# Kernel tuning notes

Hardware: AMD Instinct MI355X
Metric: run time of the kernel (lower is better)

## Reference

```python
import jax, jax.numpy as jnp
import numpy as np

B, L, D_IN = 8, 512, 1024
HEAD_SIZE = 64
NUM_LABELS = 16
INF = 1e12


def _rotary_sin_cos(seq_len, dim):
    # HF RoFormerSinusoidalPositionalEmbedding: inv_freq = 10000^(-2i/dim)
    pos = np.arange(seq_len, dtype=np.float64)[:, None]
    inv_freq = 1.0 / np.power(10000.0, 2.0 * np.arange(dim // 2) / dim)
    ang = pos * inv_freq  # [L, dim//2]
    # interleave: [s0, s0, s1, s1, ...] (matches stack([sin,sin],-1).reshape)
    sin = jnp.asarray(np.repeat(np.sin(ang), 2, axis=-1), dtype=jnp.float32)
    cos = jnp.asarray(np.repeat(np.cos(ang), 2, axis=-1), dtype=jnp.float32)
    return sin[None], cos[None]  # [1, L, dim]


def _rotate_half(x):
    # [-x1, x0, -x3, x2, ...]
    return jnp.stack([-x[..., 1::2], x[..., ::2]], axis=-1).reshape(x.shape)


def setup_inputs() -> dict:
    key = jax.random.key(0)
    k1, k2, k3, k4, k5 = jax.random.split(key, 5)
    s1 = 1.0 / np.sqrt(D_IN)
    s2 = 1.0 / np.sqrt(2 * HEAD_SIZE)
    return {
        "inputs": jax.random.normal(k1, (B, L, D_IN), dtype=jnp.float32),
        "attention_mask": jnp.ones((B, L), dtype=jnp.int32),
        "W1": jax.random.uniform(k2, (D_IN, 2 * HEAD_SIZE), jnp.float32, -s1, s1),
        "b1": jax.random.uniform(k3, (2 * HEAD_SIZE,), jnp.float32, -s1, s1),
        "W2": jax.random.uniform(k4, (2 * HEAD_SIZE, 2 * NUM_LABELS), jnp.float32, -s2, s2),
        "b2": jax.random.uniform(k5, (2 * NUM_LABELS,), jnp.float32, -s2, s2),
    }


def reference(inputs, attention_mask, W1, b1, W2, b2):
    h = inputs @ W1 + b1                      # [B, L, 2*head_size]
    qw, kw = h[..., ::2], h[..., 1::2]        # [B, L, head_size]

    sin, cos = _rotary_sin_cos(h.shape[1], HEAD_SIZE)
    qw = qw * cos + _rotate_half(qw) * sin
    kw = kw * cos + _rotate_half(kw) * sin

    logits = jnp.einsum("bmd,bnd->bmn", qw, kw) / (HEAD_SIZE ** 0.5)  # [B, L, L]

    bias = (h @ W2 + b2).transpose(0, 2, 1) / 2.0        # [B, 2*heads, L]
    logits = logits[:, None] + bias[:, ::2, None, :] + bias[:, 1::2, :, None]  # [B, heads, L, L]

    am = attention_mask.astype(logits.dtype)
    attn_mask = 1.0 - am[:, None, None, :] * am[:, None, :, None]
    logits = logits - attn_mask * INF

    tril = jnp.tril(jnp.ones((h.shape[1], h.shape[1]), logits.dtype), k=-1)
    logits = logits - tril * INF
    return logits
```

## Files before the change

kernel.cpp:

```cpp
#include <hip/hip_runtime.h>
#include <math.h>

#define B_   8
#define L_   512
#define DIN  1024
#define H_   128
#define HEAD 64
#define NL   16
#define INF_ 1.0e12f

#define SIN_OFF  0
#define COS_OFF  (512*32)
#define QROT_OFF (COS_OFF + 512*32)
#define KROT_OFF (QROT_OFF + B_*L_*HEAD)
#define BQ_OFF   (KROT_OFF + B_*L_*HEAD)
#define BK_OFF   (BQ_OFF + B_*NL*L_)
#define W1T_OFF  (BK_OFF + B_*NL*L_)
#define W2T_OFF  (W1T_OFF + 65536)

#define XSH_STRIDE 1032

typedef float          floatx4  __attribute__((ext_vector_type(4)));
typedef short          shortx8  __attribute__((ext_vector_type(8)));
typedef unsigned short ushortx8 __attribute__((ext_vector_type(8)));

__device__ __forceinline__ unsigned short f2bf(float f) {
    unsigned u = __float_as_uint(f);
    u += 0x7FFFu + ((u >> 16) & 1u);
    return (unsigned short)(u >> 16);
}

__global__ __launch_bounds__(256) void prep_kernel(const float* __restrict__ W1,
                                                   const float* __restrict__ W2,
                                                   float* __restrict__ ws) {
    __shared__ float lds[64 * 132];
    const int tid = threadIdx.x;
    const int bid = blockIdx.x;

    if (bid < 64) {
        int idx = bid * 256 + tid;
        int m = idx >> 5, i = idx & 31;
        float freq = expf(-(float)i * 0.28782313662425575f);
        float ang  = (float)m * freq;
        ws[SIN_OFF + idx] = sinf(ang);
        ws[COS_OFF + idx] = cosf(ang);
    } else if (bid < 80) {
        const int k0 = (bid - 64) * 64;
        for (int i = 0; i < 8; i++) {
            int f = tid + i * 256;
            int k = f >> 5, n4 = (f & 31) * 4;
            *(float4*)&lds[k * 132 + n4] = *(const float4*)&W1[(size_t)(k0 + k) * H_ + n4];
        }
        __syncthreads();
        unsigned short* W1T = (unsigned short*)(ws + W1T_OFF);
        const int n  = tid >> 1;
        const int kh = (tid & 1) * 32;
        for (int i = 0; i < 4; i++) {
            ushortx8 p;
            #pragma unroll
            for (int j = 0; j < 8; j++) p[j] = f2bf(lds[(kh + i * 8 + j) * 132 + n]);
            *(ushortx8*)&W1T[(size_t)n * DIN + k0 + kh + i * 8] = p;
        }
    } else {
        unsigned short* W2T = (unsigned short*)(ws + W2T_OFF);
        const int o  = tid >> 3;
        const int kc = (tid & 7) * 16;
        ushortx8 p0, p1;
        #pragma unroll
        for (int j = 0; j < 8; j++) p0[j] = f2bf(W2[(size_t)(kc + j) * 32 + o]);
        #pragma unroll
        for (int j = 0; j < 8; j++) p1[j] = f2bf(W2[(size_t)(kc + 8 + j) * 32 + o]);
        *(ushortx8*)&W2T[(size_t)o * H_ + kc]     = p0;
        *(ushortx8*)&W2T[(size_t)o * H_ + kc + 8] = p1;
    }
}

__global__ __launch_bounds__(1024, 2) void gemm1_fused_kernel(
    const float* __restrict__ X, const float* __restrict__ b1,
    const float* __restrict__ b2, float* __restrict__ ws)
{
    __shared__ __align__(16) float shbuf[8256];
    __shared__ float hs[16 * 132];

    unsigned short* Xsh = (unsigned short*)shbuf;
    float (*red)[16][64] = (float(*)[16][64])shbuf;

    const int tid  = threadIdx.x;
    const int m0   = blockIdx.x * 16;
    const int w    = tid >> 6;
    const int g    = w & 3;
    const int s    = w >> 2;
    const int lane = tid & 63;
    const int lrow = lane >> 4;
    const int lcol = lane & 15;

    const unsigned short* W1T = (const unsigned short*)(ws + W1T_OFF);

    const float* xrow = X + (size_t)(m0 + w) * DIN + lane * 8;
    float4 x0 = *(const float4*)(xrow + 0);
    float4 x1 = *(const float4*)(xrow + 4);
    float4 x2 = *(const float4*)(xrow + 512);
    float4 x3 = *(const float4*)(xrow + 516);

    const unsigned short* pB0 = W1T + (size_t)(g * 32 + lcol) * DIN + s * 256 + lrow * 8;
    const unsigned short* pB1 = pB0 + (size_t)16 * DIN;
    shortx8 bfr[16];
    #pragma unroll
    for (int st = 0; st < 8; st++) {
        bfr[2 * st]     = *(const shortx8*)(pB0 + st * 32);
        bfr[2 * st + 1] = *(const shortx8*)(pB1 + st * 32);
    }

    {
        ushortx8 ua, ub;
        ua[0] = f2bf(x0.x); ua[1] = f2bf(x0.y); ua[2] = f2bf(x0.z); ua[3] = f2bf(x0.w);
        ua[4] = f2bf(x1.x); ua[5] = f2bf(x1.y); ua[6] = f2bf(x1.z); ua[7] = f2bf(x1.w);
        ub[0] = f2bf(x2.x); ub[1] = f2bf(x2.y); ub[2] = f2bf(x2.z); ub[3] = f2bf(x2.w);
        ub[4] = f2bf(x3.x); ub[5] = f2bf(x3.y); ub[6] = f2bf(x3.z); ub[7] = f2bf(x3.w);
        *(ushortx8*)&Xsh[w * XSH_STRIDE + lane * 8]       = ua;
        *(ushortx8*)&Xsh[w * XSH_STRIDE + 512 + lane * 8] = ub;
    }
    __syncthreads();

    const unsigned short* pA = &Xsh[lcol * XSH_STRIDE + s * 256 + lrow * 8];

    floatx4 acc0 = {0.f, 0.f, 0.f, 0.f};
    floatx4 acc1 = {0.f, 0.f, 0.f, 0.f};

    #pragma unroll
    for (int st = 0; st < 8; st++) {
        shortx8 af = *(const shortx8*)(pA + st * 32);
        acc0 = __builtin_amdgcn_mfma_f32_16x16x32_bf16(af, bfr[2 * st],     acc0, 0, 0, 0);
        acc1 = __builtin_amdgcn_mfma_f32_16x16x32_bf16(af, bfr[2 * st + 1], acc1, 0, 0, 0);
    }
    __syncthreads();

    #pragma unroll
    for (int r = 0; r < 4; r++) {
        red[r][w][lane]     = acc0[r];
        red[4 + r][w][lane] = acc1[r];
    }
    __syncthreads();

    if (w < 4) {
        float b1a = b1[g * 32 + lcol];
        float b1b = b1[g * 32 + 16 + lcol];
        #pragma unroll
        for (int r = 0; r < 4; r++) {
            float v0 = red[r][g][lane]     + red[r][g + 4][lane]
                     + red[r][g + 8][lane] + red[r][g + 12][lane];
            float v1 = red[4 + r][g][lane]     + red[4 + r][g + 4][lane]
                     + red[4 + r][g + 8][lane] + red[4 + r][g + 12][lane];
            hs[(lrow * 4 + r) * 132 + g * 32 + lcol]      = v0 + b1a;
            hs[(lrow * 4 + r) * 132 + g * 32 + 16 + lcol] = v1 + b1b;
        }
    }
    __syncthreads();

    if (tid < 256) {
        int row = tid >> 4;
        int j   = tid & 15;
        int gg  = m0 + row;
        int pos = gg & (L_ - 1);
        const float* hr = &hs[row * 132];
        float h0 = hr[8 * j + 0], h1 = hr[8 * j + 1];
        float h2 = hr[8 * j + 2], h3 = hr[8 * j + 3];
        float h4 = hr[8 * j + 4], h5 = hr[8 * j + 5];
        float h6 = hr[8 * j + 6], h7 = hr[8 * j + 7];
        float s0 = ws[SIN_OFF + pos * 32 + 2 * j];
        float c0 = ws[COS_OFF + pos * 32 + 2 * j];
        float s1 = ws[SIN_OFF + pos * 32 + 2 * j + 1];
        float c1 = ws[COS_OFF + pos * 32 + 2 * j + 1];
        float4 q, k;
        q.x = h0 * c0 - h2 * s0;  q.y = h2 * c0 + h0 * s0;
        q.z = h4 * c1 - h6 * s1;  q.w = h6 * c1 + h4 * s1;
        k.x = h1 * c0 - h3 * s0;  k.y = h3 * c0 + h1 * s0;
        k.z = h5 * c1 - h7 * s1;  k.w = h7 * c1 + h5 * s1;
        *(float4*)&ws[QROT_OFF + (size_t)gg * HEAD + 4 * j] = q;
        *(float4*)&ws[KROT_OFF + (size_t)gg * HEAD + 4 * j] = k;
    }

    if (w == 0) {
        const unsigned short* W2T = (const unsigned short*)(ws + W2T_OFF);
        floatx4 bacc0 = {0.f, 0.f, 0.f, 0.f};
        floatx4 bacc1 = {0.f, 0.f, 0.f, 0.f};
        #pragma unroll
        for (int st = 0; st < 4; st++) {
            int k = st * 32 + lrow * 8;
            ushortx8 hfu;
            #pragma unroll
            for (int j = 0; j < 8; j++) hfu[j] = f2bf(hs[lcol * 132 + k + j]);
            shortx8 hf = (shortx8)hfu;
            shortx8 wf0 = *(const shortx8*)(W2T + (size_t)lcol * H_ + k);
            shortx8 wf1 = *(const shortx8*)(W2T + (size_t)(16 + lcol) * H_ + k);
            bacc0 = __builtin_amdgcn_mfma_f32_16x16x32_bf16(hf, wf0, bacc0, 0, 0, 0);
            bacc1 = __builtin_amdgcn_mfma_f32_16x16x32_bf16(hf, wf1, bacc1, 0, 0, 0);
        }
        float b2a = b2[lcol], b2b = b2[16 + lcol];
        #pragma unroll
        for (int r = 0; r < 4; r++) {
            int gg  = m0 + lrow * 4 + r;
            int bb  = gg >> 9;
            int pos = gg & (L_ - 1);
            float v0 = (bacc0[r] + b2a) * 0.5f;
            float v1 = (bacc1[r] + b2b) * 0.5f;
            int o0 = lcol, o1 = 16 + lcol;
            if (o0 & 1) ws[BQ_OFF + ((size_t)bb * NL + (o0 >> 1)) * L_ + pos] = v0;
            else        ws[BK_OFF + ((size_t)bb * NL + (o0 >> 1)) * L_ + pos] = v0;
            if (o1 & 1) ws[BQ_OFF + ((size_t)bb * NL + (o1 >> 1)) * L_ + pos] = v1;
            else        ws[BK_OFF + ((size_t)bb * NL + (o1 >> 1)) * L_ + pos] = v1;
        }
    }
}

__global__ __launch_bounds__(256) void qk_bcast_kernel(
    const int* __restrict__ am, const float* __restrict__ ws, float* __restrict__ out)
{
    __shared__ float Qs[64][68];
    __shared__ float Ks[64][68];
    __shared__ float BQs[16][64];
    __shared__ float BKs[16][64];
    __shared__ float maskM[64];
    __shared__ float maskN[64];

    const int tid = threadIdx.x;
    const int bid = blockIdx.x;
    const int bb = bid >> 6;
    const int mt = (bid >> 3) & 7;
    const int nt = bid & 7;
    const int m0 = mt * 64, n0 = nt * 64;

    {
        int r0   = tid >> 4;
        int dcol = (tid & 15) * 4;
        #pragma unroll
        for (int rr = 0; rr < 4; rr++) {
            int r = r0 + rr * 16;
            float4 q = *(const float4*)&ws[QROT_OFF + ((size_t)(bb * L_ + m0 + r)) * HEAD + dcol];
            float4 k = *(const float4*)&ws[KROT_OFF + ((size_t)(bb * L_ + n0 + r)) * HEAD + dcol];
            Qs[dcol + 0][r] = q.x; Qs[dcol + 1][r] = q.y;
            Qs[dcol + 2][r] = q.z; Qs[dcol + 3][r] = q.w;
            Ks[dcol + 0][r] = k.x; Ks[dcol + 1][r] = k.y;
            Ks[dcol + 2][r] = k.z; Ks[dcol + 3][r] = k.w;
        }
    }
    {
        int l = tid >> 4;
        int c = (tid & 15) * 4;
        *(float4*)&BQs[l][c] = *(const float4*)&ws[BQ_OFF + ((size_t)bb * NL + l) * L_ + m0 + c];
        *(float4*)&BKs[l][c] = *(const float4*)&ws[BK_OFF + ((size_t)bb * NL + l) * L_ + n0 + c];
    }
    if (tid < 64)       maskM[tid]      = (float)am[bb * L_ + m0 + tid];
    else if (tid < 128) maskN[tid - 64] = (float)am[bb * L_ + n0 + (tid - 64)];
    __syncthreads();

    const int ty = tid >> 4;
    const int tx = tid & 15;
    float acc[4][4] = {};
    #pragma unroll 8
    for (int d = 0; d < HEAD; d++) {
        float4 a  = *(const float4*)&Qs[d][ty * 4];
        float4 bv = *(const float4*)&Ks[d][tx * 4];
        acc[0][0] += a.x * bv.x; acc[0][1] += a.x * bv.y; acc[0][2] += a.x * bv.z; acc[0][3] += a.x * bv.w;
        acc[1][0] += a.y * bv.x; acc[1][1] += a.y * bv.y; acc[1][2] += a.y * bv.z; acc[1][3] += a.y * bv.w;
        acc[2][0] += a.z * bv.x; acc[2][1] += a.z * bv.y; acc[2][2] += a.z * bv.z; acc[2][3] += a.z * bv.w;
        acc[3][0] += a.w * bv.x; acc[3][1] += a.w * bv.y; acc[3][2] += a.w * bv.z; acc[3][3] += a.w * bv.w;
    }

    float4 base[4];
    #pragma unroll
    for (int r = 0; r < 4; r++) {
        int m = m0 + ty * 4 + r;
        float mm = maskM[ty * 4 + r];
        #pragma unroll
        for (int c = 0; c < 4; c++) {
            int n = n0 + tx * 4 + c;
            float v = acc[r][c] * 0.125f
                    - (1.0f - mm * maskN[tx * 4 + c]) * INF_
                    - ((n < m) ? INF_ : 0.0f);
            ((float*)&base[r])[c] = v;
        }
    }

    #pragma unroll
    for (int l = 0; l < NL; l++) {
        float4 bk4 = *(const float4*)&BKs[l][tx * 4];
        size_t outb = (((size_t)(bb * NL + l)) * L_ + m0 + ty * 4) * L_ + n0 + tx * 4;
        #pragma unroll
        for (int r = 0; r < 4; r++) {
            float bq = BQs[l][ty * 4 + r];
            float4 o;
            o.x = base[r].x + bk4.x + bq;
            o.y = base[r].y + bk4.y + bq;
            o.z = base[r].z + bk4.z + bq;
            o.w = base[r].w + bk4.w + bq;
            *(float4*)&out[outb + (size_t)r * L_] = o;
        }
    }
}

extern "C" void kernel_launch(void* const* d_in, const int* in_sizes, int n_in,
                              void* d_out, int out_size, void* d_ws, size_t ws_size,
                              hipStream_t stream) {
    const float* X  = (const float*)d_in[0];
    const int*   am = (const int*)d_in[1];
    const float* W1 = (const float*)d_in[2];
    const float* b1 = (const float*)d_in[3];
    const float* W2 = (const float*)d_in[4];
    const float* b2 = (const float*)d_in[5];
    float* out = (float*)d_out;
    float* ws  = (float*)d_ws;

    prep_kernel<<<81, 256, 0, stream>>>(W1, W2, ws);
    gemm1_fused_kernel<<<(B_ * L_) / 16, 1024, 0, stream>>>(X, b1, b2, ws);
    qk_bcast_kernel<<<B_ * (L_ / 64) * (L_ / 64), 256, 0, stream>>>(am, ws, out);
}
```

Measured before the change: 48.48 us.

## Split first GEMM into split-K partial kernel plus separate reduction epilogue

Replaces the single 1024-thread fused GEMM kernel with a 1024-block split-K kernel that writes partial sums to workspace. A new epilogue kernel sums the partials, adds bias, applies rotary, and computes the bias projection in FP32 from shared memory. This drops the W2 bf16 transpose from prep. The aim is more, smaller blocks for better occupancy, at the cost of an extra launch and a global round-trip for the partials.

New measurement: 55.72 us. 14.9% more time.

```diff
diff --git a/kernel.cpp b/kernel.cpp
--- a/kernel.cpp
+++ b/kernel.cpp
@@ -16,9 +16,7 @@
 #define BQ_OFF   (KROT_OFF + B_*L_*HEAD)
 #define BK_OFF   (BQ_OFF + B_*NL*L_)
 #define W1T_OFF  (BK_OFF + B_*NL*L_)
-#define W2T_OFF  (W1T_OFF + 65536)
-
-#define XSH_STRIDE 1032
+#define PART_OFF (W1T_OFF + 65536)
 
 typedef float          floatx4  __attribute__((ext_vector_type(4)));
 typedef short          shortx8  __attribute__((ext_vector_type(8)));
@@ -31,7 +29,6 @@
 }
 
 __global__ __launch_bounds__(256) void prep_kernel(const float* __restrict__ W1,
-                                                   const float* __restrict__ W2,
                                                    float* __restrict__ ws) {
     __shared__ float lds[64 * 132];
     const int tid = threadIdx.x;
@@ -44,7 +41,7 @@
         float ang  = (float)m * freq;
         ws[SIN_OFF + idx] = sinf(ang);
         ws[COS_OFF + idx] = cosf(ang);
-    } else if (bid < 80) {
+    } else {
         const int k0 = (bid - 64) * 64;
         for (int i = 0; i < 8; i++) {
             int f = tid + i * 256;
@@ -61,48 +58,35 @@
             for (int j = 0; j < 8; j++) p[j] = f2bf(lds[(kh + i * 8 + j) * 132 + n]);
             *(ushortx8*)&W1T[(size_t)n * DIN + k0 + kh + i * 8] = p;
         }
-    } else {
-        unsigned short* W2T = (unsigned short*)(ws + W2T_OFF);
-        const int o  = tid >> 3;
-        const int kc = (tid & 7) * 16;
-        ushortx8 p0, p1;
-        #pragma unroll
-        for (int j = 0; j < 8; j++) p0[j] = f2bf(W2[(size_t)(kc + j) * 32 + o]);
-        #pragma unroll
-        for (int j = 0; j < 8; j++) p1[j] = f2bf(W2[(size_t)(kc + 8 + j) * 32 + o]);
-        *(ushortx8*)&W2T[(size_t)o * H_ + kc]     = p0;
-        *(ushortx8*)&W2T[(size_t)o * H_ + kc + 8] = p1;
-    }
-}
-
-__global__ __launch_bounds__(1024, 2) void gemm1_fused_kernel(
-    const float* __restrict__ X, const float* __restrict__ b1,
-    const float* __restrict__ b2, float* __restrict__ ws)
+    }
+}
+
+__global__ __launch_bounds__(256, 4) void gemm1_partial_kernel(
+    const float* __restrict__ X, float* __restrict__ ws)
 {
-    __shared__ __align__(16) float shbuf[8256];
-    __shared__ float hs[16 * 132];
-
-    unsigned short* Xsh = (unsigned short*)shbuf;
-    float (*red)[16][64] = (float(*)[16][64])shbuf;
+    __shared__ __align__(16) unsigned short Xsh[16][264];
 
     const int tid  = threadIdx.x;
-    const int m0   = blockIdx.x * 16;
+    const int bid  = blockIdx.x;
+    const int mt   = bid >> 2;
+    const int ks   = bid & 3;
+    const int m0   = mt * 16;
+    const int k0   = ks * 256;
     const int w    = tid >> 6;
-    const int g    = w & 3;
-    const int s    = w >> 2;
     const int lane = tid & 63;
     const int lrow = lane >> 4;
     const int lcol = lane & 15;
 
     const unsigned short* W1T = (const unsigned short*)(ws + W1T_OFF);
 
-    const float* xrow = X + (size_t)(m0 + w) * DIN + lane * 8;
-    float4 x0 = *(const float4*)(xrow + 0);
-    float4 x1 = *(const float4*)(xrow + 4);
-    float4 x2 = *(const float4*)(xrow + 512);
-    float4 x3 = *(const float4*)(xrow + 516);
-
-    const unsigned short* pB0 = W1T + (size_t)(g * 32 + lcol) * DIN + s * 256 + lrow * 8;
+    const int xr = 4 * w + lrow;
+    const float* src = X + (size_t)(m0 + xr) * DIN + k0 + lcol * 16;
+    float4 v0 = *(const float4*)(src + 0);
+    float4 v1 = *(const float4*)(src + 4);
+    float4 v2 = *(const float4*)(src + 8);
+    float4 v3 = *(const float4*)(src + 12);
+
+    const unsigned short* pB0 = W1T + (size_t)(w * 32 + lcol) * DIN + k0 + lrow * 8;
     const unsigned short* pB1 = pB0 + (size_t)16 * DIN;
     shortx8 bfr[16];
     #pragma unroll
@@ -113,51 +97,72 @@
 
     {
         ushortx8 ua, ub;
-        ua[0] = f2bf(x0.x); ua[1] = f2bf(x0.y); ua[2] = f2bf(x0.z); ua[3] = f2bf(x0.w);
-        ua[4] = f2bf(x1.x); ua[5] = f2bf(x1.y); ua[6] = f2bf(x1.z); ua[7] = f2bf(x1.w);
-        ub[0] = f2bf(x2.x); ub[1] = f2bf(x2.y); ub[2] = f2bf(x2.z); ub[3] = f2bf(x2.w);
-        ub[4] = f2bf(x3.x); ub[5] = f2bf(x3.y); ub[6] = f2bf(x3.z); ub[7] = f2bf(x3.w);
-        *(ushortx8*)&Xsh[w * XSH_STRIDE + lane * 8]       = ua;
-        *(ushortx8*)&Xsh[w * XSH_STRIDE + 512 + lane * 8] = ub;
+        ua[0] = f2bf(v0.x); ua[1] = f2bf(v0.y); ua[2] = f2bf(v0.z); ua[3] = f2bf(v0.w);
+        ua[4] = f2bf(v1.x); ua[5] = f2bf(v1.y); ua[6] = f2bf(v1.z); ua[7] = f2bf(v1.w);
+        ub[0] = f2bf(v2.x); ub[1] = f2bf(v2.y); ub[2] = f2bf(v2.z); ub[3] = f2bf(v2.w);
+        ub[4] = f2bf(v3.x); ub[5] = f2bf(v3.y); ub[6] = f2bf(v3.z); ub[7] = f2bf(v3.w);
+        *(ushortx8*)&Xsh[xr][lcol * 16]     = ua;
+        *(ushortx8*)&Xsh[xr][lcol * 16 + 8] = ub;
     }
     __syncthreads();
-
-    const unsigned short* pA = &Xsh[lcol * XSH_STRIDE + s * 256 + lrow * 8];
 
     floatx4 acc0 = {0.f, 0.f, 0.f, 0.f};
     floatx4 acc1 = {0.f, 0.f, 0.f, 0.f};
-
     #pragma unroll
     for (int st = 0; st < 8; st++) {
-        shortx8 af = *(const shortx8*)(pA + st * 32);
+        shortx8 af = *(const shortx8*)&Xsh[lcol][st * 32 + lrow * 8];
         acc0 = __builtin_amdgcn_mfma_f32_16x16x32_bf16(af, bfr[2 * st],     acc0, 0, 0, 0);
         acc1 = __builtin_amdgcn_mfma_f32_16x16x32_bf16(af, bfr[2 * st + 1], acc1, 0, 0, 0);
     }
+
+    float* part = ws + PART_OFF + ((size_t)(mt * 4 + ks)) * 2048;
+    #pragma unroll
+    for (int r = 0; r < 4; r++) {
+        part[(lrow * 4 + r) * 128 + w * 32 + lcol]      = acc0[r];
+        part[(lrow * 4 + r) * 128 + w * 32 + 16 + lcol] = acc1[r];
+    }
+}
+
+__global__ __launch_bounds__(256) void epilogue_kernel(
+    const float* __restrict__ W2, const float* __restrict__ b1,
+    const float* __restrict__ b2, float* __restrict__ ws)
+{
+    __shared__ float hs[16 * 132];
+    __shared__ float W2s[4096];
+
+    const int tid = threadIdx.x;
+    const int mt  = blockIdx.x;
+    const int m0  = mt * 16;
+
+    {
+        const float4* wsrc = (const float4*)W2;
+        float4* wdst = (float4*)W2s;
+        #pragma unroll
+        for (int i = 0; i < 4; i++) wdst[tid + i * 256] = wsrc[tid + i * 256];
+    }
+
+    {
+        const float* p = ws + PART_OFF + (size_t)mt * 4 * 2048 + tid * 8;
+        float4 s0 = *(const float4*)(p + 0);
+        float4 s1 = *(const float4*)(p + 4);
+        #pragma unroll
+        for (int k = 1; k < 4; k++) {
+            float4 a0 = *(const float4*)(p + k * 2048 + 0);
+            float4 a1 = *(const float4*)(p + k * 2048 + 4);
+            s0.x += a0.x; s0.y += a0.y; s0.z += a0.z; s0.w += a0.w;
+            s1.x += a1.x; s1.y += a1.y; s1.z += a1.z; s1.w += a1.w;
+        }
+        int row = tid >> 4, col = (tid & 15) * 8;
+        float4 bb0 = *(const float4*)(b1 + col);
+        float4 bb1 = *(const float4*)(b1 + col + 4);
+        s0.x += bb0.x; s0.y += bb0.y; s0.z += bb0.z; s0.w += bb0.w;
+        s1.x += bb1.x; s1.y += bb1.y; s1.z += bb1.z; s1.w += bb1.w;
+        *(float4*)&hs[row * 132 + col]     = s0;
+        *(float4*)&hs[row * 132 + col + 4] = s1;
+    }
     __syncthreads();
 
-    #pragma unroll
-    for (int r = 0; r < 4; r++) {
-        red[r][w][lane]     = acc0[r];
-        red[4 + r][w][lane] = acc1[r];
-    }
-    __syncthreads();
-
-    if (w < 4) {
-        float b1a = b1[g * 32 + lcol];
-        float b1b = b1[g * 32 + 16 + lcol];
-        #pragma unroll
-        for (int r = 0; r < 4; r++) {
-            float v0 = red[r][g][lane]     + red[r][g + 4][lane]
-                     + red[r][g + 8][lane] + red[r][g + 12][lane];
-            float v1 = red[4 + r][g][lane]     + red[4 + r][g + 4][lane]
-                     + red[4 + r][g + 8][lane] + red[4 + r][g + 12][lane];
-            hs[(lrow * 4 + r) * 132 + g * 32 + lcol]      = v0 + b1a;
-            hs[(lrow * 4 + r) * 132 + g * 32 + 16 + lcol] = v1 + b1b;
-        }
-    }
-    __syncthreads();
-
-    if (tid < 256) {
+    {
         int row = tid >> 4;
         int j   = tid & 15;
         int gg  = m0 + row;
@@ -180,36 +185,26 @@
         *(float4*)&ws[KROT_OFF + (size_t)gg * HEAD + 4 * j] = k;
     }
 
-    if (w == 0) {
-        const unsigned short* W2T = (const unsigned short*)(ws + W2T_OFF);
-        floatx4 bacc0 = {0.f, 0.f, 0.f, 0.f};
-        floatx4 bacc1 = {0.f, 0.f, 0.f, 0.f};
-        #pragma unroll
-        for (int st = 0; st < 4; st++) {
-            int k = st * 32 + lrow * 8;
-            ushortx8 hfu;
-            #pragma unroll
-            for (int j = 0; j < 8; j++) hfu[j] = f2bf(hs[lcol * 132 + k + j]);
-            shortx8 hf = (shortx8)hfu;
-            shortx8 wf0 = *(const shortx8*)(W2T + (size_t)lcol * H_ + k);
-            shortx8 wf1 = *(const shortx8*)(W2T + (size_t)(16 + lcol) * H_ + k);
-            bacc0 = __builtin_amdgcn_mfma_f32_16x16x32_bf16(hf, wf0, bacc0, 0, 0, 0);
-            bacc1 = __builtin_amdgcn_mfma_f32_16x16x32_bf16(hf, wf1, bacc1, 0, 0, 0);
-        }
-        float b2a = b2[lcol], b2b = b2[16 + lcol];
-        #pragma unroll
-        for (int r = 0; r < 4; r++) {
-            int gg  = m0 + lrow * 4 + r;
-            int bb  = gg >> 9;
-            int pos = gg & (L_ - 1);
-            float v0 = (bacc0[r] + b2a) * 0.5f;
-            float v1 = (bacc1[r] + b2b) * 0.5f;
-            int o0 = lcol, o1 = 16 + lcol;
-            if (o0 & 1) ws[BQ_OFF + ((size_t)bb * NL + (o0 >> 1)) * L_ + pos] = v0;
-            else        ws[BK_OFF + ((size_t)bb * NL + (o0 >> 1)) * L_ + pos] = v0;
-            if (o1 & 1) ws[BQ_OFF + ((size_t)bb * NL + (o1 >> 1)) * L_ + pos] = v1;
-            else        ws[BK_OFF + ((size_t)bb * NL + (o1 >> 1)) * L_ + pos] = v1;
-        }
+    #pragma unroll
+    for (int half = 0; half < 2; half++) {
+        int idx = tid + half * 256;
+        int row = idx >> 5;
+        int o   = idx & 31;
+        float sum = b2[o];
+        const float* hr = &hs[row * 132];
+        #pragma unroll
+        for (int c = 0; c < H_; c += 4) {
+            sum += hr[c + 0] * W2s[(c + 0) * 32 + o]
+                 + hr[c + 1] * W2s[(c + 1) * 32 + o]
+                 + hr[c + 2] * W2s[(c + 2) * 32 + o]
+                 + hr[c + 3] * W2s[(c + 3) * 32 + o];
+        }
+        sum *= 0.5f;
+        int gg  = m0 + row;
+        int bb  = gg >> 9;
+        int pos = gg & (L_ - 1);
+        if (o & 1) ws[BQ_OFF + ((size_t)bb * NL + (o >> 1)) * L_ + pos] = sum;
+        else       ws[BK_OFF + ((size_t)bb * NL + (o >> 1)) * L_ + pos] = sum;
     }
 }
 
@@ -311,7 +306,8 @@
     float* out = (float*)d_out;
     float* ws  = (float*)d_ws;
 
-    prep_kernel<<<81, 256, 0, stream>>>(W1, W2, ws);
-    gemm1_fused_kernel<<<(B_ * L_) / 16, 1024, 0, stream>>>(X, b1, b2, ws);
+    prep_kernel<<<80, 256, 0, stream>>>(W1, ws);
+    gemm1_partial_kernel<<<1024, 256, 0, stream>>>(X, ws);
+    epilogue_kernel<<<256, 256, 0, stream>>>(W2, b1, b2, ws);
     qk_bcast_kernel<<<B_ * (L_ / 64) * (L_ / 64), 256, 0, stream>>>(am, ws, out);
 }
```
